# Kernel optimization log

Measured on AMD Instinct MI355X. Metric: run time of the kernel, lower is better.

Reference implementation:

```python
import jax, jax.numpy as jnp
import numpy as np

N_NODES = 100000


def gcn_conv(x, edge_index, W, b):
    # PyG GCNConv: add self-loops, symmetric normalization D^-1/2 (A+I) D^-1/2, transform, aggregate, bias.
    src, dst = edge_index[0], edge_index[1]
    n = x.shape[0]
    xw = x @ W  # [N, out] transform before propagate (PyG order)
    # degree with self-loops (count edges by target + 1)
    deg = jax.ops.segment_sum(jnp.ones_like(dst, dtype=xw.dtype), dst, num_segments=n) + 1.0
    dinv = jax.lax.rsqrt(deg)  # deg >= 1, safe
    norm = dinv[src] * dinv[dst]  # [E]
    msgs = xw[src] * norm[:, None]  # [E, out] gathered, normalized messages
    agg = jax.ops.segment_sum(msgs, dst, num_segments=n)
    # self-loop contribution: norm_ii = dinv_i^2 = 1/deg_i
    agg = agg + xw * (dinv * dinv)[:, None]
    return agg + b


def setup_inputs() -> dict:
    key = jax.random.key(0)
    ks = jax.random.split(key, 8)
    in_c, h1, h2, out_c = 128, 71, 82, 1
    x = jax.random.normal(ks[0], (N_NODES, in_c), dtype=jnp.float32)
    edge_index = jax.random.randint(ks[1], (2, 1600000), 0, N_NODES, dtype=jnp.int64)
    def glorot(k, fan_in, fan_out):
        s = jnp.sqrt(6.0 / (fan_in + fan_out))
        return jax.random.uniform(k, (fan_in, fan_out), jnp.float32, -s, s)
    return {
        "x": x,
        "edge_index": edge_index,
        "W1": glorot(ks[2], in_c, h1), "b1": jnp.zeros((h1,), jnp.float32),
        "W2": glorot(ks[3], h1, h2), "b2": jnp.zeros((h2,), jnp.float32),
        "W3": glorot(ks[4], h2, out_c), "b3": jnp.zeros((out_c,), jnp.float32),
    }


def reference(x, edge_index, W1, b1, W2, b2, W3, b3):
    h = jax.nn.relu(gcn_conv(x, edge_index, W1, b1))
    h = gcn_conv(h, edge_index, W2, b2)  # note: no relu after conv2 in source
    return gcn_conv(h, edge_index, W3, b3)
```

## Files before the change

### kernel.cpp

```cpp
#include <hip/hip_runtime.h>
#include <hip/hip_fp16.h>

#define NNODES 100000
#define NB 196
#define BSHIFT 9
#define BMASK 511
#define BCAP 9216
#define WT_LD 136

typedef _Float16 half8 __attribute__((ext_vector_type(8)));
typedef float floatx4 __attribute__((ext_vector_type(4)));

__global__ void binA_kernel(const int* __restrict__ src, const int* __restrict__ dst,
                            int* __restrict__ bcnt, unsigned* __restrict__ bdata, int E) {
    __shared__ int hist[NB];
    __shared__ int gb[NB];
    __shared__ int cur[NB];
    const int BATCH = 4096;
    for (int base = blockIdx.x * BATCH; base < E; base += gridDim.x * BATCH) {
        for (int i = threadIdx.x; i < NB; i += blockDim.x) hist[i] = 0;
        __syncthreads();
        int s[16], d[16];
        int cnt = 0;
        if (base + BATCH <= E) {
#pragma unroll
            for (int q = 0; q < 4; ++q) {
                int4 sv = ((const int4*)(src + base))[q * 256 + threadIdx.x];
                int4 dv = ((const int4*)(dst + base))[q * 256 + threadIdx.x];
                s[cnt] = sv.x; d[cnt] = dv.x; atomicAdd(&hist[dv.x >> BSHIFT], 1); ++cnt;
                s[cnt] = sv.y; d[cnt] = dv.y; atomicAdd(&hist[dv.y >> BSHIFT], 1); ++cnt;
                s[cnt] = sv.z; d[cnt] = dv.z; atomicAdd(&hist[dv.z >> BSHIFT], 1); ++cnt;
                s[cnt] = sv.w; d[cnt] = dv.w; atomicAdd(&hist[dv.w >> BSHIFT], 1); ++cnt;
            }
        } else {
#pragma unroll
            for (int k = 0; k < 16; ++k) {
                int idx = base + k * 256 + threadIdx.x;
                if (idx < E) {
                    s[cnt] = src[idx];
                    d[cnt] = dst[idx];
                    atomicAdd(&hist[d[cnt] >> BSHIFT], 1);
                    ++cnt;
                }
            }
        }
        __syncthreads();
        for (int i = threadIdx.x; i < NB; i += blockDim.x) {
            int c = hist[i];
            gb[i] = (c > 0) ? atomicAdd(&bcnt[i], c) : 0;
            cur[i] = 0;
        }
        __syncthreads();
        for (int k = 0; k < cnt; ++k) {
            int b = d[k] >> BSHIFT;
            int lo = gb[b] + atomicAdd(&cur[b], 1);
            if (lo < BCAP)
                bdata[(size_t)b * BCAP + lo] = ((unsigned)s[k] << BSHIFT) | ((unsigned)d[k] & BMASK);
        }
        __syncthreads();
    }
}

__global__ __launch_bounds__(1024) void prep_kernel(
        const int* __restrict__ bcnt, int* __restrict__ bstart,
        const float* __restrict__ W2, const float* __restrict__ b2,
        const float* __restrict__ W3, float* __restrict__ w23,
        const float* __restrict__ W1, __half* __restrict__ Wt) {
    if (blockIdx.x == 0) {
        __shared__ int sh[NB];
        int t = threadIdx.x;
        if (t < NB) sh[t] = min(bcnt[t], BCAP);
        __syncthreads();
        if (t == 0) {
            int acc = 0;
            for (int i = 0; i < NB; ++i) { int v = sh[i]; sh[i] = acc; acc += v; }
        }
        __syncthreads();
        if (t < NB) bstart[t] = sh[t];
    } else if (blockIdx.x == 1) {
        int k = threadIdx.x;
        if (k < 71) {
            float a = 0.f;
            for (int j = 0; j < 82; ++j) a += W2[k * 82 + j] * W3[j];
            w23[k] = a;
        } else if (k == 71) {
            float a = 0.f;
            for (int j = 0; j < 82; ++j) a += b2[j] * W3[j];
            w23[71] = a;
        }
    } else {
        for (int i = threadIdx.x; i < 80 * WT_LD; i += blockDim.x) {
            int nn = i / WT_LD, k = i - nn * WT_LD;
            float v = (nn < 71 && k < 128) ? W1[k * 71 + nn] : 0.f;
            Wt[i] = __float2half(v);
        }
    }
}

__global__ __launch_bounds__(1024) void binB2_kernel(
        const int* __restrict__ bcnt, const int* __restrict__ bstart,
        const unsigned* __restrict__ bdata,
        int* __restrict__ deg, int* __restrict__ end_off, float* __restrict__ dinv,
        int* __restrict__ csr, int n) {
    __shared__ unsigned edata[BCAP];
    __shared__ int hist[512];
    __shared__ int cur[512];
    __shared__ int wsum[8];
    int b = blockIdx.x;
    int tid = threadIdx.x;
    int cnt = min(bcnt[b], BCAP);
    int base = bstart[b];
    const unsigned* p = bdata + (size_t)b * BCAP;
    if (tid < 512) hist[tid] = 0;
    __syncthreads();
    for (int i = tid; i < cnt; i += 1024) {
        unsigned e = p[i];
        edata[i] = e;
        atomicAdd(&hist[e & BMASK], 1);
    }
    __syncthreads();
    if (tid < 512) {
        int v = hist[tid];
        int lane = tid & 63;
        int incl = v;
#pragma unroll
        for (int off = 1; off < 64; off <<= 1) {
            int t = __shfl_up(incl, off);
            if (lane >= off) incl += t;
        }
        cur[tid] = incl;
        if (lane == 63) wsum[tid >> 6] = incl;
    }
    __syncthreads();
    if (tid == 0) {
        int acc = 0;
#pragma unroll
        for (int w = 0; w < 8; ++w) { int t = wsum[w]; wsum[w] = acc; acc += t; }
    }
    __syncthreads();
    if (tid < 512) {
        int v = hist[tid];
        int start = base + wsum[tid >> 6] + cur[tid] - v;
        int node = (b << BSHIFT) + tid;
        if (node < n) {
            deg[node] = v;
            end_off[node] = start + v;
            dinv[node] = rsqrtf((float)v + 1.0f);
        }
        cur[tid] = start;
    }
    __syncthreads();
    for (int i = tid; i < cnt; i += 1024) {
        unsigned e = edata[i];
        int pos = atomicAdd(&cur[e & BMASK], 1);
        csr[pos] = (int)(e >> BSHIFT);
    }
}

__global__ __launch_bounds__(256) void xform_mfma(
        const float* __restrict__ x, const __half* __restrict__ Wt,
        const float* __restrict__ scale, __half* __restrict__ msg, int n) {
    __shared__ __half Wsh[80 * WT_LD];
    {
        const uint4* sp = (const uint4*)Wt;
        uint4* dp = (uint4*)Wsh;
        for (int i = threadIdx.x; i < (80 * WT_LD * 2) / 16; i += blockDim.x) dp[i] = sp[i];
    }
    __syncthreads();
    int lane = threadIdx.x & 63;
    int m = lane & 15, q = lane >> 4;
    int gw = (blockIdx.x * blockDim.x + threadIdx.x) >> 6;
    int nw = (gridDim.x * blockDim.x) >> 6;
    int nrt = n >> 4;
    for (int rt = gw; rt < nrt; rt += nw) {
        int rb = rt << 4;
        const float* xr = x + (size_t)(rb + m) * 128 + q * 8;
        floatx4 acc[5];
#pragma unroll
        for (int t = 0; t < 5; ++t) acc[t] = (floatx4){0.f, 0.f, 0.f, 0.f};
#pragma unroll
        for (int ks = 0; ks < 4; ++ks) {
            float4 f0 = *(const float4*)(xr + ks * 32);
            float4 f1 = *(const float4*)(xr + ks * 32 + 4);
            half8 a;
            a[0] = (_Float16)f0.x; a[1] = (_Float16)f0.y;
            a[2] = (_Float16)f0.z; a[3] = (_Float16)f0.w;
            a[4] = (_Float16)f1.x; a[5] = (_Float16)f1.y;
            a[6] = (_Float16)f1.z; a[7] = (_Float16)f1.w;
#pragma unroll
            for (int t = 0; t < 5; ++t) {
                half8 b = *(const half8*)&Wsh[(t * 16 + m) * WT_LD + ks * 32 + q * 8];
                acc[t] = __builtin_amdgcn_mfma_f32_16x16x32_f16(a, b, acc[t], 0, 0, 0);
            }
        }
        float sc[4];
#pragma unroll
        for (int r = 0; r < 4; ++r) sc[r] = scale[rb + q * 4 + r];
#pragma unroll
        for (int t = 0; t < 5; ++t) {
            int col = t * 16 + m;
            if (col < 72) {
#pragma unroll
                for (int r = 0; r < 4; ++r)
                    msg[(size_t)(rb + q * 4 + r) * 72 + col] = __float2half(acc[t][r] * sc[r]);
            }
        }
    }
}

template <int OC>
__global__ void gather_fused(const __half2* __restrict__ msg, const int* __restrict__ csr,
                             const int* __restrict__ end_off, const int* __restrict__ deg,
                             const float* __restrict__ dinv, const float* __restrict__ b,
                             const float* __restrict__ w23, float* __restrict__ g2, int n) {
    constexpr int OC2 = (OC + 1) / 2;
    int lane = threadIdx.x & 63;
    int wid = (blockIdx.x * blockDim.x + threadIdx.x) >> 6;
    int nwaves = (gridDim.x * blockDim.x) >> 6;
    bool act = lane < OC2;
    int c = lane << 1;
    float bx = (act && c < OC) ? b[c] : 0.f;
    float by = (act && c + 1 < OC) ? b[c + 1] : 0.f;
    float w0 = (act && c < OC) ? w23[c] : 0.f;
    float w1 = (act && c + 1 < OC) ? w23[c + 1] : 0.f;
    for (int node = wid; node < n; node += nwaves) {
        int end = end_off[node];
        int cnt = deg[node];
        int start = end - cnt;
        float ax0 = 0.f, ay0 = 0.f, ax1 = 0.f, ay1 = 0.f;
        float ax2 = 0.f, ay2 = 0.f, ax3 = 0.f, ay3 = 0.f;
        for (int base = 0; base < cnt; base += 64) {
            int rem = min(cnt - base, 64);
            int se = (lane < rem) ? csr[start + base + lane] : 0;
            int j = 0;
            for (; j + 15 < rem; j += 16) {
                int s0  = __builtin_amdgcn_readlane(se, j + 0);
                int s1  = __builtin_amdgcn_readlane(se, j + 1);
                int s2  = __builtin_amdgcn_readlane(se, j + 2);
                int s3  = __builtin_amdgcn_readlane(se, j + 3);
                int s4  = __builtin_amdgcn_readlane(se, j + 4);
                int s5  = __builtin_amdgcn_readlane(se, j + 5);
                int s6  = __builtin_amdgcn_readlane(se, j + 6);
                int s7  = __builtin_amdgcn_readlane(se, j + 7);
                int s8  = __builtin_amdgcn_readlane(se, j + 8);
                int s9  = __builtin_amdgcn_readlane(se, j + 9);
                int s10 = __builtin_amdgcn_readlane(se, j + 10);
                int s11 = __builtin_amdgcn_readlane(se, j + 11);
                int s12 = __builtin_amdgcn_readlane(se, j + 12);
                int s13 = __builtin_amdgcn_readlane(se, j + 13);
                int s14 = __builtin_amdgcn_readlane(se, j + 14);
                int s15 = __builtin_amdgcn_readlane(se, j + 15);
                if (act) {
                    float2 v0  = __half22float2(msg[(size_t)s0  * OC2 + lane]);
                    float2 v1  = __half22float2(msg[(size_t)s1  * OC2 + lane]);
                    float2 v2  = __half22float2(msg[(size_t)s2  * OC2 + lane]);
                    float2 v3  = __half22float2(msg[(size_t)s3  * OC2 + lane]);
                    float2 v4  = __half22float2(msg[(size_t)s4  * OC2 + lane]);
                    float2 v5  = __half22float2(msg[(size_t)s5  * OC2 + lane]);
                    float2 v6  = __half22float2(msg[(size_t)s6  * OC2 + lane]);
                    float2 v7  = __half22float2(msg[(size_t)s7  * OC2 + lane]);
                    float2 v8  = __half22float2(msg[(size_t)s8  * OC2 + lane]);
                    float2 v9  = __half22float2(msg[(size_t)s9  * OC2 + lane]);
                    float2 v10 = __half22float2(msg[(size_t)s10 * OC2 + lane]);
                    float2 v11 = __half22float2(msg[(size_t)s11 * OC2 + lane]);
                    float2 v12 = __half22float2(msg[(size_t)s12 * OC2 + lane]);
                    float2 v13 = __half22float2(msg[(size_t)s13 * OC2 + lane]);
                    float2 v14 = __half22float2(msg[(size_t)s14 * OC2 + lane]);
                    float2 v15 = __half22float2(msg[(size_t)s15 * OC2 + lane]);
                    ax0 += v0.x;  ay0 += v0.y;   ax1 += v1.x;  ay1 += v1.y;
                    ax2 += v2.x;  ay2 += v2.y;   ax3 += v3.x;  ay3 += v3.y;
                    ax0 += v4.x;  ay0 += v4.y;   ax1 += v5.x;  ay1 += v5.y;
                    ax2 += v6.x;  ay2 += v6.y;   ax3 += v7.x;  ay3 += v7.y;
                    ax0 += v8.x;  ay0 += v8.y;   ax1 += v9.x;  ay1 += v9.y;
                    ax2 += v10.x; ay2 += v10.y;  ax3 += v11.x; ay3 += v11.y;
                    ax0 += v12.x; ay0 += v12.y;  ax1 += v13.x; ay1 += v13.y;
                    ax2 += v14.x; ay2 += v14.y;  ax3 += v15.x; ay3 += v15.y;
                }
            }
            for (; j + 7 < rem; j += 8) {
                int s0 = __builtin_amdgcn_readlane(se, j + 0);
                int s1 = __builtin_amdgcn_readlane(se, j + 1);
                int s2 = __builtin_amdgcn_readlane(se, j + 2);
                int s3 = __builtin_amdgcn_readlane(se, j + 3);
                int s4 = __builtin_amdgcn_readlane(se, j + 4);
                int s5 = __builtin_amdgcn_readlane(se, j + 5);
                int s6 = __builtin_amdgcn_readlane(se, j + 6);
                int s7 = __builtin_amdgcn_readlane(se, j + 7);
                if (act) {
                    float2 v0 = __half22float2(msg[(size_t)s0 * OC2 + lane]);
                    float2 v1 = __half22float2(msg[(size_t)s1 * OC2 + lane]);
                    float2 v2 = __half22float2(msg[(size_t)s2 * OC2 + lane]);
                    float2 v3 = __half22float2(msg[(size_t)s3 * OC2 + lane]);
                    float2 v4 = __half22float2(msg[(size_t)s4 * OC2 + lane]);
                    float2 v5 = __half22float2(msg[(size_t)s5 * OC2 + lane]);
                    float2 v6 = __half22float2(msg[(size_t)s6 * OC2 + lane]);
                    float2 v7 = __half22float2(msg[(size_t)s7 * OC2 + lane]);
                    ax0 += v0.x; ay0 += v0.y;  ax1 += v1.x; ay1 += v1.y;
                    ax2 += v2.x; ay2 += v2.y;  ax3 += v3.x; ay3 += v3.y;
                    ax0 += v4.x; ay0 += v4.y;  ax1 += v5.x; ay1 += v5.y;
                    ax2 += v6.x; ay2 += v6.y;  ax3 += v7.x; ay3 += v7.y;
                }
            }
            for (; j + 3 < rem; j += 4) {
                int s0 = __builtin_amdgcn_readlane(se, j + 0);
                int s1 = __builtin_amdgcn_readlane(se, j + 1);
                int s2 = __builtin_amdgcn_readlane(se, j + 2);
                int s3 = __builtin_amdgcn_readlane(se, j + 3);
                if (act) {
                    float2 v0 = __half22float2(msg[(size_t)s0 * OC2 + lane]);
                    float2 v1 = __half22float2(msg[(size_t)s1 * OC2 + lane]);
                    float2 v2 = __half22float2(msg[(size_t)s2 * OC2 + lane]);
                    float2 v3 = __half22float2(msg[(size_t)s3 * OC2 + lane]);
                    ax0 += v0.x; ay0 += v0.y;  ax1 += v1.x; ay1 += v1.y;
                    ax2 += v2.x; ay2 += v2.y;  ax3 += v3.x; ay3 += v3.y;
                }
            }
            for (; j < rem; ++j) {
                int s = __builtin_amdgcn_readlane(se, j);
                if (act) {
                    float2 v = __half22float2(msg[(size_t)s * OC2 + lane]);
                    ax0 += v.x; ay0 += v.y;
                }
            }
        }
        float dv = dinv[node];
        float p = 0.f;
        if (act) {
            float2 selfv = __half22float2(msg[(size_t)node * OC2 + lane]);
            float sx = ((ax0 + ax1) + (ax2 + ax3)) + selfv.x;
            float sy = ((ay0 + ay1) + (ay2 + ay3)) + selfv.y;
            float vx = fmaxf(dv * sx + bx, 0.f);
            float vy = fmaxf(dv * sy + by, 0.f);
            p = vx * w0 + vy * w1;
        }
#pragma unroll
        for (int off = 32; off > 0; off >>= 1) p += __shfl_down(p, off);
        if (lane == 0) g2[node] = dv * p;
    }
}

__global__ void sgather_q(const float* __restrict__ g2, const int* __restrict__ csr,
                          const int* __restrict__ end_off, const int* __restrict__ deg,
                          const float* __restrict__ dinv, const float* __restrict__ w23,
                          float* __restrict__ q, int n) {
    float bw = w23[71];
    int lane = threadIdx.x & 63;
    int g = lane >> 4, k = lane & 15;
    int wid = (blockIdx.x * blockDim.x + threadIdx.x) >> 6;
    int nw = (gridDim.x * blockDim.x) >> 6;
    for (int i0 = wid * 4; i0 < n; i0 += nw * 4) {
        int i = i0 + g;
        float acc = 0.f;
        float dv = 0.f;
        if (i < n) {
            int end = end_off[i];
            int cnt = deg[i];
            int start = end - cnt;
            dv = dinv[i];
            for (int e = k; e < cnt; e += 16) acc += g2[csr[start + e]];
        }
        acc += __shfl_down(acc, 8, 16);
        acc += __shfl_down(acc, 4, 16);
        acc += __shfl_down(acc, 2, 16);
        acc += __shfl_down(acc, 1, 16);
        if (i < n && k == 0) q[i] = dv * (dv * (acc + g2[i]) + bw);
    }
}

__global__ void sgather_out(const float* __restrict__ q, const int* __restrict__ csr,
                            const int* __restrict__ end_off, const int* __restrict__ deg,
                            const float* __restrict__ dinv, const float* __restrict__ b3,
                            float* __restrict__ out, int n) {
    float bv = b3[0];
    int lane = threadIdx.x & 63;
    int g = lane >> 4, k = lane & 15;
    int wid = (blockIdx.x * blockDim.x + threadIdx.x) >> 6;
    int nw = (gridDim.x * blockDim.x) >> 6;
    for (int i0 = wid * 4; i0 < n; i0 += nw * 4) {
        int i = i0 + g;
        float acc = 0.f;
        float dv = 0.f;
        if (i < n) {
            int end = end_off[i];
            int cnt = deg[i];
            int start = end - cnt;
            dv = dinv[i];
            for (int e = k; e < cnt; e += 16) acc += q[csr[start + e]];
        }
        acc += __shfl_down(acc, 8, 16);
        acc += __shfl_down(acc, 4, 16);
        acc += __shfl_down(acc, 2, 16);
        acc += __shfl_down(acc, 1, 16);
        if (i < n && k == 0) out[i] = dv * (acc + q[i]) + bv;
    }
}

extern "C" void kernel_launch(void* const* d_in, const int* in_sizes, int n_in,
                              void* d_out, int out_size, void* d_ws, size_t ws_size,
                              hipStream_t stream) {
    const float* x  = (const float*)d_in[0];
    const int*   ei = (const int*)d_in[1];
    const float* W1 = (const float*)d_in[2];
    const float* b1 = (const float*)d_in[3];
    const float* W2 = (const float*)d_in[4];
    const float* b2 = (const float*)d_in[5];
    const float* W3 = (const float*)d_in[6];
    const float* b3 = (const float*)d_in[7];
    float* out = (float*)d_out;

    const int n = NNODES;
    const int E = in_sizes[1] / 2;
    const int* src = ei;
    const int* dst = ei + E;

    float* ws     = (float*)d_ws;
    float* dinv   = ws;
    int*   deg_i  = (int*)(ws + n);
    int*   offs   = deg_i + n;
    int*   bcnt   = offs + n;
    int*   bstart = bcnt + 256;
    float* w23    = (float*)(bstart + 256);
    __half* Wt    = (__half*)(w23 + 80);
    float* g2     = (float*)(Wt + 11008);
    float* q      = g2 + n;
    int*   csr    = (int*)(q + n);
    __half* msg   = (__half*)(csr + E);
    unsigned* bdata = (unsigned*)(msg + (size_t)n * 72);

    hipMemsetAsync(bcnt, 0, 256 * sizeof(int), stream);
    binA_kernel<<<(E + 4095) / 4096, 256, 0, stream>>>(src, dst, bcnt, bdata, E);
    prep_kernel<<<3, 1024, 0, stream>>>(bcnt, bstart, W2, b2, W3, w23, W1, Wt);
    binB2_kernel<<<NB, 1024, 0, stream>>>(bcnt, bstart, bdata, deg_i, offs, dinv, csr, n);

    xform_mfma<<<1563, 256, 0, stream>>>(x, Wt, dinv, msg, n);

    gather_fused<71><<<2048, 256, 0, stream>>>((const __half2*)msg, csr, offs, deg_i, dinv, b1, w23, g2, n);

    sgather_q<<<1024, 256, 0, stream>>>(g2, csr, offs, deg_i, dinv, w23, q, n);
    sgather_out<<<1024, 256, 0, stream>>>(q, csr, offs, deg_i, dinv, b3, out, n);
}
```

Before: 240.6 us.

## Split message rows into 128B and 16B arrays, gather two neighbors per wave

The transformed features, previously stored as 72-half rows, are split into a 64-column array (exactly 128 bytes per row) and an 8-column tail array. The gather kernel now has each half-wave fetch a different neighbor's 128-byte row, so all 64 lanes are active instead of 36. The tail columns are fetched separately with 16 neighbors per wave-load, and partial sums are combined with cross-lane shuffles. This aims at better lane utilization and aligned row accesses, at the cost of extra shuffles, a second scattered load stream and slightly more index bookkeeping.

```diff
diff --git a/kernel.cpp b/kernel.cpp
--- a/kernel.cpp
+++ b/kernel.cpp
@@ -159,7 +159,8 @@
 
 __global__ __launch_bounds__(256) void xform_mfma(
         const float* __restrict__ x, const __half* __restrict__ Wt,
-        const float* __restrict__ scale, __half* __restrict__ msg, int n) {
+        const float* __restrict__ scale, __half* __restrict__ msgA,
+        __half* __restrict__ msgB, int n) {
     __shared__ __half Wsh[80 * WT_LD];
     {
         const uint4* sp = (const uint4*)Wt;
@@ -199,143 +200,116 @@
 #pragma unroll
         for (int t = 0; t < 5; ++t) {
             int col = t * 16 + m;
-            if (col < 72) {
-#pragma unroll
-                for (int r = 0; r < 4; ++r)
-                    msg[(size_t)(rb + q * 4 + r) * 72 + col] = __float2half(acc[t][r] * sc[r]);
-            }
-        }
-    }
-}
-
-template <int OC>
-__global__ void gather_fused(const __half2* __restrict__ msg, const int* __restrict__ csr,
-                             const int* __restrict__ end_off, const int* __restrict__ deg,
-                             const float* __restrict__ dinv, const float* __restrict__ b,
-                             const float* __restrict__ w23, float* __restrict__ g2, int n) {
-    constexpr int OC2 = (OC + 1) / 2;
+#pragma unroll
+            for (int r = 0; r < 4; ++r) {
+                __half hv = __float2half(acc[t][r] * sc[r]);
+                int row = rb + q * 4 + r;
+                if (t < 4) {
+                    msgA[(size_t)row * 64 + col] = hv;
+                } else if (m < 8) {
+                    msgB[(size_t)row * 8 + m] = hv;
+                }
+            }
+        }
+    }
+}
+
+__global__ __launch_bounds__(256) void gather_fused(
+        const __half2* __restrict__ msgA, const __half2* __restrict__ msgB,
+        const int* __restrict__ csr, const int* __restrict__ end_off,
+        const int* __restrict__ deg, const float* __restrict__ dinv,
+        const float* __restrict__ b, const float* __restrict__ w23,
+        float* __restrict__ g2, int n) {
     int lane = threadIdx.x & 63;
     int wid = (blockIdx.x * blockDim.x + threadIdx.x) >> 6;
     int nwaves = (gridDim.x * blockDim.x) >> 6;
-    bool act = lane < OC2;
-    int c = lane << 1;
-    float bx = (act && c < OC) ? b[c] : 0.f;
-    float by = (act && c + 1 < OC) ? b[c + 1] : 0.f;
-    float w0 = (act && c < OC) ? w23[c] : 0.f;
-    float w1 = (act && c + 1 < OC) ? w23[c + 1] : 0.f;
+    int k = lane & 31;
+    int c = k << 1;
+    float bxA = b[c], byA = b[c + 1];
+    float w0A = w23[c], w1A = w23[c + 1];
+    int p = lane & 3;
+    int cb = 64 + (p << 1);
+    float bxB = b[cb];
+    float byB = (cb + 1 < 71) ? b[cb + 1] : 0.f;
+    float w0B = w23[cb];
+    float w1B = (cb + 1 < 71) ? w23[cb + 1] : 0.f;
+    const char* mA = (const char*)msgA;
+    const char* mB = (const char*)msgB;
+    unsigned laneOffA = (unsigned)(k << 2);
+    unsigned laneOffB = (unsigned)(p << 2);
     for (int node = wid; node < n; node += nwaves) {
         int end = end_off[node];
         int cnt = deg[node];
         int start = end - cnt;
         float ax0 = 0.f, ay0 = 0.f, ax1 = 0.f, ay1 = 0.f;
         float ax2 = 0.f, ay2 = 0.f, ax3 = 0.f, ay3 = 0.f;
+        float bxs = 0.f, bys = 0.f;
         for (int base = 0; base < cnt; base += 64) {
             int rem = min(cnt - base, 64);
             int se = (lane < rem) ? csr[start + base + lane] : 0;
             int j = 0;
-            for (; j + 15 < rem; j += 16) {
-                int s0  = __builtin_amdgcn_readlane(se, j + 0);
-                int s1  = __builtin_amdgcn_readlane(se, j + 1);
-                int s2  = __builtin_amdgcn_readlane(se, j + 2);
-                int s3  = __builtin_amdgcn_readlane(se, j + 3);
-                int s4  = __builtin_amdgcn_readlane(se, j + 4);
-                int s5  = __builtin_amdgcn_readlane(se, j + 5);
-                int s6  = __builtin_amdgcn_readlane(se, j + 6);
-                int s7  = __builtin_amdgcn_readlane(se, j + 7);
-                int s8  = __builtin_amdgcn_readlane(se, j + 8);
-                int s9  = __builtin_amdgcn_readlane(se, j + 9);
-                int s10 = __builtin_amdgcn_readlane(se, j + 10);
-                int s11 = __builtin_amdgcn_readlane(se, j + 11);
-                int s12 = __builtin_amdgcn_readlane(se, j + 12);
-                int s13 = __builtin_amdgcn_readlane(se, j + 13);
-                int s14 = __builtin_amdgcn_readlane(se, j + 14);
-                int s15 = __builtin_amdgcn_readlane(se, j + 15);
-                if (act) {
-                    float2 v0  = __half22float2(msg[(size_t)s0  * OC2 + lane]);
-                    float2 v1  = __half22float2(msg[(size_t)s1  * OC2 + lane]);
-                    float2 v2  = __half22float2(msg[(size_t)s2  * OC2 + lane]);
-                    float2 v3  = __half22float2(msg[(size_t)s3  * OC2 + lane]);
-                    float2 v4  = __half22float2(msg[(size_t)s4  * OC2 + lane]);
-                    float2 v5  = __half22float2(msg[(size_t)s5  * OC2 + lane]);
-                    float2 v6  = __half22float2(msg[(size_t)s6  * OC2 + lane]);
-                    float2 v7  = __half22float2(msg[(size_t)s7  * OC2 + lane]);
-                    float2 v8  = __half22float2(msg[(size_t)s8  * OC2 + lane]);
-                    float2 v9  = __half22float2(msg[(size_t)s9  * OC2 + lane]);
-                    float2 v10 = __half22float2(msg[(size_t)s10 * OC2 + lane]);
-                    float2 v11 = __half22float2(msg[(size_t)s11 * OC2 + lane]);
-                    float2 v12 = __half22float2(msg[(size_t)s12 * OC2 + lane]);
-                    float2 v13 = __half22float2(msg[(size_t)s13 * OC2 + lane]);
-                    float2 v14 = __half22float2(msg[(size_t)s14 * OC2 + lane]);
-                    float2 v15 = __half22float2(msg[(size_t)s15 * OC2 + lane]);
-                    ax0 += v0.x;  ay0 += v0.y;   ax1 += v1.x;  ay1 += v1.y;
-                    ax2 += v2.x;  ay2 += v2.y;   ax3 += v3.x;  ay3 += v3.y;
-                    ax0 += v4.x;  ay0 += v4.y;   ax1 += v5.x;  ay1 += v5.y;
-                    ax2 += v6.x;  ay2 += v6.y;   ax3 += v7.x;  ay3 += v7.y;
-                    ax0 += v8.x;  ay0 += v8.y;   ax1 += v9.x;  ay1 += v9.y;
-                    ax2 += v10.x; ay2 += v10.y;  ax3 += v11.x; ay3 += v11.y;
-                    ax0 += v12.x; ay0 += v12.y;  ax1 += v13.x; ay1 += v13.y;
-                    ax2 += v14.x; ay2 += v14.y;  ax3 += v15.x; ay3 += v15.y;
-                }
-            }
             for (; j + 7 < rem; j += 8) {
-                int s0 = __builtin_amdgcn_readlane(se, j + 0);
-                int s1 = __builtin_amdgcn_readlane(se, j + 1);
-                int s2 = __builtin_amdgcn_readlane(se, j + 2);
-                int s3 = __builtin_amdgcn_readlane(se, j + 3);
-                int s4 = __builtin_amdgcn_readlane(se, j + 4);
-                int s5 = __builtin_amdgcn_readlane(se, j + 5);
-                int s6 = __builtin_amdgcn_readlane(se, j + 6);
-                int s7 = __builtin_amdgcn_readlane(se, j + 7);
-                if (act) {
-                    float2 v0 = __half22float2(msg[(size_t)s0 * OC2 + lane]);
-                    float2 v1 = __half22float2(msg[(size_t)s1 * OC2 + lane]);
-                    float2 v2 = __half22float2(msg[(size_t)s2 * OC2 + lane]);
-                    float2 v3 = __half22float2(msg[(size_t)s3 * OC2 + lane]);
-                    float2 v4 = __half22float2(msg[(size_t)s4 * OC2 + lane]);
-                    float2 v5 = __half22float2(msg[(size_t)s5 * OC2 + lane]);
-                    float2 v6 = __half22float2(msg[(size_t)s6 * OC2 + lane]);
-                    float2 v7 = __half22float2(msg[(size_t)s7 * OC2 + lane]);
-                    ax0 += v0.x; ay0 += v0.y;  ax1 += v1.x; ay1 += v1.y;
-                    ax2 += v2.x; ay2 += v2.y;  ax3 += v3.x; ay3 += v3.y;
-                    ax0 += v4.x; ay0 += v4.y;  ax1 += v5.x; ay1 += v5.y;
-                    ax2 += v6.x; ay2 += v6.y;  ax3 += v7.x; ay3 += v7.y;
-                }
-            }
-            for (; j + 3 < rem; j += 4) {
-                int s0 = __builtin_amdgcn_readlane(se, j + 0);
-                int s1 = __builtin_amdgcn_readlane(se, j + 1);
-                int s2 = __builtin_amdgcn_readlane(se, j + 2);
-                int s3 = __builtin_amdgcn_readlane(se, j + 3);
-                if (act) {
-                    float2 v0 = __half22float2(msg[(size_t)s0 * OC2 + lane]);
-                    float2 v1 = __half22float2(msg[(size_t)s1 * OC2 + lane]);
-                    float2 v2 = __half22float2(msg[(size_t)s2 * OC2 + lane]);
-                    float2 v3 = __half22float2(msg[(size_t)s3 * OC2 + lane]);
-                    ax0 += v0.x; ay0 += v0.y;  ax1 += v1.x; ay1 += v1.y;
-                    ax2 += v2.x; ay2 += v2.y;  ax3 += v3.x; ay3 += v3.y;
-                }
-            }
-            for (; j < rem; ++j) {
+                int sa0 = __builtin_amdgcn_readlane(se, j + 0);
+                int sb0 = __builtin_amdgcn_readlane(se, j + 1);
+                int sa1 = __builtin_amdgcn_readlane(se, j + 2);
+                int sb1 = __builtin_amdgcn_readlane(se, j + 3);
+                int sa2 = __builtin_amdgcn_readlane(se, j + 4);
+                int sb2 = __builtin_amdgcn_readlane(se, j + 5);
+                int sa3 = __builtin_amdgcn_readlane(se, j + 6);
+                int sb3 = __builtin_amdgcn_readlane(se, j + 7);
+                int s0 = (lane < 32) ? sa0 : sb0;
+                int s1 = (lane < 32) ? sa1 : sb1;
+                int s2 = (lane < 32) ? sa2 : sb2;
+                int s3 = (lane < 32) ? sa3 : sb3;
+                float2 v0 = __half22float2(*(const __half2*)(mA + (((unsigned)s0 << 7) | laneOffA)));
+                float2 v1 = __half22float2(*(const __half2*)(mA + (((unsigned)s1 << 7) | laneOffA)));
+                float2 v2 = __half22float2(*(const __half2*)(mA + (((unsigned)s2 << 7) | laneOffA)));
+                float2 v3 = __half22float2(*(const __half2*)(mA + (((unsigned)s3 << 7) | laneOffA)));
+                ax0 += v0.x; ay0 += v0.y;  ax1 += v1.x; ay1 += v1.y;
+                ax2 += v2.x; ay2 += v2.y;  ax3 += v3.x; ay3 += v3.y;
+            }
+            for (; j + 1 < rem; j += 2) {
+                int sa = __builtin_amdgcn_readlane(se, j);
+                int sb = __builtin_amdgcn_readlane(se, j + 1);
+                int s = (lane < 32) ? sa : sb;
+                float2 v = __half22float2(*(const __half2*)(mA + (((unsigned)s << 7) | laneOffA)));
+                ax0 += v.x; ay0 += v.y;
+            }
+            if (j < rem) {
                 int s = __builtin_amdgcn_readlane(se, j);
-                if (act) {
-                    float2 v = __half22float2(msg[(size_t)s * OC2 + lane]);
-                    ax0 += v.x; ay0 += v.y;
-                }
-            }
+                float2 v = __half22float2(*(const __half2*)(mA + (((unsigned)s << 7) | laneOffA)));
+                if (lane < 32) { ax0 += v.x; ay0 += v.y; }
+            }
+            for (int t = 0; t < rem; t += 16) {
+                int idx = t + (lane >> 2);
+                int ss = __shfl(se, (idx < rem) ? idx : (rem - 1));
+                float2 v = __half22float2(*(const __half2*)(mB + (((unsigned)ss << 4) | laneOffB)));
+                if (idx < rem) { bxs += v.x; bys += v.y; }
+            }
+        }
+        float axA = (ax0 + ax1) + (ax2 + ax3);
+        float ayA = (ay0 + ay1) + (ay2 + ay3);
+        axA += __shfl_xor(axA, 32);
+        ayA += __shfl_xor(ayA, 32);
+        {
+            float2 sv = __half22float2(msgA[(size_t)node * 32 + k]);
+            axA += sv.x; ayA += sv.y;
+        }
+        bxs += __shfl_xor(bxs, 4);  bxs += __shfl_xor(bxs, 8);
+        bxs += __shfl_xor(bxs, 16); bxs += __shfl_xor(bxs, 32);
+        bys += __shfl_xor(bys, 4);  bys += __shfl_xor(bys, 8);
+        bys += __shfl_xor(bys, 16); bys += __shfl_xor(bys, 32);
+        {
+            float2 sv = __half22float2(msgB[(size_t)node * 4 + p]);
+            bxs += sv.x; bys += sv.y;
         }
         float dv = dinv[node];
-        float p = 0.f;
-        if (act) {
-            float2 selfv = __half22float2(msg[(size_t)node * OC2 + lane]);
-            float sx = ((ax0 + ax1) + (ax2 + ax3)) + selfv.x;
-            float sy = ((ay0 + ay1) + (ay2 + ay3)) + selfv.y;
-            float vx = fmaxf(dv * sx + bx, 0.f);
-            float vy = fmaxf(dv * sy + by, 0.f);
-            p = vx * w0 + vy * w1;
-        }
-#pragma unroll
-        for (int off = 32; off > 0; off >>= 1) p += __shfl_down(p, off);
-        if (lane == 0) g2[node] = dv * p;
+        float pa = fmaxf(dv * axA + bxA, 0.f) * w0A + fmaxf(dv * ayA + byA, 0.f) * w1A;
+        float pb = fmaxf(dv * bxs + bxB, 0.f) * w0B + fmaxf(dv * bys + byB, 0.f) * w1B;
+        float r = ((lane < 32) ? pa : 0.f) + ((lane < 4) ? pb : 0.f);
+#pragma unroll
+        for (int off = 32; off > 0; off >>= 1) r += __shfl_down(r, off);
+        if (lane == 0) g2[node] = dv * r;
     }
 }
 
@@ -424,17 +398,19 @@
     float* g2     = (float*)(Wt + 11008);
     float* q      = g2 + n;
     int*   csr    = (int*)(q + n);
-    __half* msg   = (__half*)(csr + E);
-    unsigned* bdata = (unsigned*)(msg + (size_t)n * 72);
+    __half* msgA  = (__half*)(csr + E + 16);
+    __half* msgB  = msgA + (size_t)n * 64;
+    unsigned* bdata = (unsigned*)(msgB + (size_t)n * 8);
 
     hipMemsetAsync(bcnt, 0, 256 * sizeof(int), stream);
     binA_kernel<<<(E + 4095) / 4096, 256, 0, stream>>>(src, dst, bcnt, bdata, E);
     prep_kernel<<<3, 1024, 0, stream>>>(bcnt, bstart, W2, b2, W3, w23, W1, Wt);
     binB2_kernel<<<NB, 1024, 0, stream>>>(bcnt, bstart, bdata, deg_i, offs, dinv, csr, n);
 
-    xform_mfma<<<1563, 256, 0, stream>>>(x, Wt, dinv, msg, n);
-
-    gather_fused<71><<<2048, 256, 0, stream>>>((const __half2*)msg, csr, offs, deg_i, dinv, b1, w23, g2, n);
+    xform_mfma<<<1563, 256, 0, stream>>>(x, Wt, dinv, msgA, msgB, n);
+
+    gather_fused<<<2048, 256, 0, stream>>>((const __half2*)msgA, (const __half2*)msgB,
+                                           csr, offs, deg_i, dinv, b1, w23, g2, n);
 
     sgather_q<<<1024, 256, 0, stream>>>(g2, csr, offs, deg_i, dinv, w23, q, n);
     sgather_out<<<1024, 256, 0, stream>>>(q, csr, offs, deg_i, dinv, b3, out, n);
```

Result: no change. 238.9 us (-0.7%).
